# Kernel optimization log

Measured on AMD Instinct MI355X. Metric: run time of the kernel, lower is better.

The kernel has to match this reference:

```python
import jax, jax.numpy as jnp
import numpy as np

HEAD_DIM = 128
N_HEADS = 16
N_KV_HEADS = 4
ROPE_BASE = 10000.0
TRAIN_SEQ_LEN = 1024


def _rotary_cos_sin(seq_len, rd, base=ROPE_BASE, train_len=TRAIN_SEQ_LEN):
    # NTK-style base scaling when seq_len exceeds training length (matches Rotary.forward)
    if seq_len > train_len:
        scale = seq_len / train_len
        base = base * scale ** (rd / (rd - 2))
    inv_freq = 1.0 / base ** (np.arange(0, rd, 2, dtype=np.float32) / rd)
    freqs = np.outer(np.arange(seq_len, dtype=np.float32), inv_freq)  # [T, rd/2]
    cos = jnp.asarray(np.cos(freqs))[None, :, None, :]  # [1,T,1,rd/2]
    sin = jnp.asarray(np.sin(freqs))[None, :, None, :]
    return cos, sin


def _apply_rotary(x, cos, sin):
    h = x.shape[-1] // 2
    x1, x2 = x[..., :h], x[..., h:]
    return jnp.concatenate((x1 * cos + x2 * sin, -x1 * sin + x2 * cos), axis=-1)


def _rms_norm(x):
    eps = jnp.finfo(x.dtype).eps
    return x * jax.lax.rsqrt(jnp.mean(x * x, axis=-1, keepdims=True) + eps)


def setup_inputs() -> dict:
    key = jax.random.key(0)
    ks = jax.random.split(key, 6)
    B, T, D = 4, 2048, 2048
    x = jax.random.normal(ks[0], (B, T, D), dtype=jnp.float32)
    q_w = jax.random.normal(ks[1], (D, D), dtype=jnp.float32) * 0.02
    k_w = jax.random.normal(ks[2], (N_KV_HEADS * HEAD_DIM, D), dtype=jnp.float32) * 0.02
    v_w = jax.random.normal(ks[3], (N_KV_HEADS * HEAD_DIM, D), dtype=jnp.float32) * 0.02
    out_w = jax.random.normal(ks[4], (D, D), dtype=jnp.float32) * 0.02
    q_gain = jnp.ones((N_HEADS,), dtype=jnp.float32)
    return {"x": x, "q_w": q_w, "k_w": k_w, "v_w": v_w, "out_w": out_w, "q_gain": q_gain}


def reference(x, q_w, k_w, v_w, out_w, q_gain):
    B, T, D = x.shape
    q = (x @ q_w.T).reshape(B, T, N_HEADS, HEAD_DIM)
    k = (x @ k_w.T).reshape(B, T, N_KV_HEADS, HEAD_DIM)
    v = (x @ v_w.T).reshape(B, T, N_KV_HEADS, HEAD_DIM)
    q = _rms_norm(q)
    k = _rms_norm(k)
    cos, sin = _rotary_cos_sin(T, HEAD_DIM)
    q = _apply_rotary(q, cos, sin)
    k = _apply_rotary(k, cos, sin)
    q = q * q_gain[None, None, :, None]
    # GQA: expand kv heads (repeat_interleave semantics)
    rep = N_HEADS // N_KV_HEADS
    k = jnp.repeat(k, rep, axis=2)  # [B,T,H,D]
    v = jnp.repeat(v, rep, axis=2)
    scale = 1.0 / jnp.sqrt(jnp.asarray(HEAD_DIM, dtype=x.dtype))
    scores = jnp.einsum("bthd,bshd->bhts", q, k) * scale  # [B,H,T,T]
    causal = jnp.tril(jnp.ones((T, T), dtype=bool))
    scores = jnp.where(causal[None, None], scores, jnp.asarray(-jnp.inf, dtype=scores.dtype))
    w = jax.nn.softmax(scores, axis=-1)
    y = jnp.einsum("bhts,bshd->bthd", w, v).reshape(B, T, D)
    return y @ out_w.T
```

## Files before the change

### kernel.cpp

```cpp
#include <hip/hip_runtime.h>
#include <hip/hip_bf16.h>
#include <math.h>

#define HEAD_DIM 128
#define NH 16
#define NKV 4
#define BB 4
#define TT 2048
#define DD 2048
#define ROWS (BB*TT)

typedef unsigned short u16;
typedef unsigned int u32;
typedef __attribute__((ext_vector_type(8))) short short8;
typedef __attribute__((ext_vector_type(4))) float f32x4;
typedef __attribute__((ext_vector_type(16))) float f32x16;
typedef __attribute__((ext_vector_type(4))) unsigned short u16x4;

__device__ __forceinline__ float bf2f(u16 u) {
    union { unsigned int i; float f; } v; v.i = ((unsigned int)u) << 16; return v.f;
}
__device__ __forceinline__ u16 f2bf(float f) {
    union { float f; unsigned int i; } v; v.f = f;
    unsigned int r = v.i + 0x7FFFu + ((v.i >> 16) & 1u);
    return (u16)(r >> 16);
}
__device__ __forceinline__ f32x4 mfma16(short8 a, short8 b, f32x4 c) {
    return __builtin_amdgcn_mfma_f32_16x16x32_bf16(a, b, c, 0, 0, 0);
}
__device__ __forceinline__ f32x16 mfma32(short8 a, short8 b, f32x16 c) {
    return __builtin_amdgcn_mfma_f32_32x32x16_bf16(a, b, c, 0, 0, 0);
}
__device__ __forceinline__ f32x16 zero16() {
    f32x16 z;
    #pragma unroll
    for (int i = 0; i < 16; ++i) z[i] = 0.f;
    return z;
}
__device__ __forceinline__ void gload_lds16(const u16* g, u16* l) {
    __builtin_amdgcn_global_load_lds(
        (const __attribute__((address_space(1))) unsigned int*)(const void*)g,
        (__attribute__((address_space(3))) unsigned int*)(void*)l, 16, 0, 0);
}

__global__ __launch_bounds__(256)
void cast_f2b(const float* __restrict__ in, u16* __restrict__ out, int n)
{
    int i = (blockIdx.x * 256 + threadIdx.x) * 4;
    if (i >= n) return;
    float4 v = *(const float4*)(in + i);
    u16x4 o;
    o.x = f2bf(v.x); o.y = f2bf(v.y); o.z = f2bf(v.z); o.w = f2bf(v.w);
    *(u16x4*)(out + i) = o;
}

__global__ __launch_bounds__(256)
void rope_table(float* __restrict__ cs, float* __restrict__ sn, float base)
{
    int idx = blockIdx.x * 256 + threadIdx.x;
    if (idx >= TT * 64) return;
    int t = idx >> 6;
    int d = idx & 63;
    float inv = powf(base, -(float)(2 * d) / 128.0f);
    float f = (float)t * inv;
    cs[idx] = cosf(f);
    sn[idx] = sinf(f);
}

__global__ __launch_bounds__(256)
void rmsrope_bf16(const u16* __restrict__ xin, u16* __restrict__ xout,
                  const float* __restrict__ cs, const float* __restrict__ sn,
                  const float* __restrict__ gain,
                  int heads, int use_gain, float pre, int relayout)
{
    int row  = blockIdx.x * 4 + (threadIdx.x >> 6);
    int lane = threadIdx.x & 63;
    int h = row % heads;
    int t = (row / heads) % TT;
    int b = row / (heads * TT);
    size_t base = (size_t)row * HEAD_DIM;

    float x1 = bf2f(xin[base + lane]);
    float x2 = bf2f(xin[base + 64 + lane]);
    float ss = x1 * x1 + x2 * x2;
    #pragma unroll
    for (int m = 1; m < 64; m <<= 1) ss += __shfl_xor(ss, m, 64);
    float r = 1.0f / sqrtf(ss * (1.0f / 128.0f) + 1.1920929e-7f);
    x1 *= r; x2 *= r;

    float c = cs[t * 64 + lane];
    float s = sn[t * 64 + lane];
    float o1 =  x1 * c + x2 * s;
    float o2 = -x1 * s + x2 * c;
    float g = use_gain ? gain[h] * pre : pre;
    o1 *= g; o2 *= g;

    size_t orow = relayout ? ((size_t)(b * heads + h) * TT + t) : (size_t)row;
    size_t obase = orow * HEAD_DIM;
    xout[obase + lane]      = f2bf(o1);
    xout[obase + 64 + lane] = f2bf(o2);
}

__global__ __launch_bounds__(256)
void transpose_v(const u16* __restrict__ vbh, u16* __restrict__ vtb)
{
    __shared__ u16 tile[64][72];
    const int tb = blockIdx.x;
    const int db = blockIdx.y;
    const int z  = blockIdx.z;
    const int tid = threadIdx.x;

    {
        const int r = tid >> 2, cq = tid & 3;
        const u16* src = vbh + ((size_t)(((z >> 2) * TT + tb * 64 + r) * NKV + (z & 3))) * 128
                             + db * 64 + cq * 16;
        short8 s0 = *(const short8*)(src);
        short8 s1 = *(const short8*)(src + 8);
        #pragma unroll
        for (int e = 0; e < 8; ++e) tile[r][cq * 16 + e]     = (u16)s0[e];
        #pragma unroll
        for (int e = 0; e < 8; ++e) tile[r][cq * 16 + 8 + e] = (u16)s1[e];
    }
    __syncthreads();
    {
        const int d = tid >> 2, tq = tid & 3;
        __attribute__((aligned(16))) u16 tmp[16];
        #pragma unroll
        for (int e = 0; e < 16; ++e) {
            int esw = (e & 3) | ((e & 4) << 1) | ((e & 8) >> 1);
            tmp[e] = tile[tq * 16 + esw][d];
        }
        u16* dst = vtb + (((size_t)(z * (TT / 64) + tb) * 128 + (db * 64 + d)) << 6) + tq * 16;
        *(short8*)(dst)     = ((short8*)tmp)[0];
        *(short8*)(dst + 8) = ((short8*)tmp)[1];
    }
}

template<int BN, int OUTMODE>
__global__ __launch_bounds__(512, 2)
void gemm256(const u16* __restrict__ A, const u16* __restrict__ W,
             void* __restrict__ C0, void* __restrict__ C1)
{
    constexpr int WN    = (BN == 256) ? 4 : 2;
    constexpr int MR    = (BN == 256) ? 8 : 4;
    constexpr int WROW  = (BN == 256) ? 128 : 64;
    constexpr int NT    = DD / 64;
    constexpr int BROWS = BN / 8;
    constexpr int NBI   = BROWS / 8;

    __shared__ u16 AsL[2 * 256 * 64];
    __shared__ u16 BsL[2 * BN * 64];

    const int tid = threadIdx.x;
    const int w = tid >> 6, l = tid & 63;
    const int lq = l & 15, lg = l >> 4;
    const int wmi = (WN == 4) ? (w >> 2) : (w >> 1);
    const int wni = w & (WN - 1);

    int bmi, bni;
    {
        const int bid = blockIdx.x;
        const int wg = (bid & 7) * 32 + (bid >> 3);
        const int st = wg >> 2, wi = wg & 3;
        const int sty = st >> 2, stx = st & 3;
        bmi = sty * 2 + (wi >> 1);
        bni = stx * 2 + (wi & 1);
    }
    const int bm = bmi * 256, bn = bni * BN;

    const int r8 = l >> 3;
    const int chs = (l & 7) ^ r8;
    const u16* Ag = A + (size_t)(bm + r8) * DD + chs * 8;
    const u16* Wg = W + (size_t)(bn + r8) * DD + chs * 8;

    f32x4 acc[MR][4];
    #pragma unroll
    for (int m = 0; m < MR; ++m)
        #pragma unroll
        for (int n = 0; n < 4; ++n) acc[m][n] = (f32x4){0.f, 0.f, 0.f, 0.f};

    auto stage = [&](int buf, int t) {
        const size_t ko = (size_t)t * 64;
        u16* Ad = AsL + buf * (256 * 64);
        u16* Bd = BsL + buf * (BN * 64);
        #pragma unroll
        for (int j = 0; j < 4; ++j) {
            int rb = w * 32 + j * 8;
            gload_lds16(Ag + (size_t)rb * DD + ko, Ad + rb * 64);
        }
        #pragma unroll
        for (int j = 0; j < NBI; ++j) {
            int rb = w * BROWS + j * 8;
            gload_lds16(Wg + (size_t)rb * DD + ko, Bd + rb * 64);
        }
    };

    stage(0, 0);
    stage(1, 1);
    if constexpr (BN == 256) asm volatile("s_waitcnt vmcnt(8)" ::: "memory");
    else                     asm volatile("s_waitcnt vmcnt(6)" ::: "memory");
    __builtin_amdgcn_s_barrier();
    __builtin_amdgcn_sched_barrier(0);

    const int swz = lq & 7;
    for (int t = 0; t < NT; ++t) {
        const int buf = t & 1;
        const u16* Ab = AsL + buf * (256 * 64);
        const u16* Bb = BsL + buf * (BN * 64);
        #pragma unroll
        for (int ks = 0; ks < 2; ++ks) {
            short8 af[MR], bf[4];
            #pragma unroll
            for (int m = 0; m < MR; ++m) {
                int arow = wmi * WROW + m * 16 + lq;
                af[m] = *(const short8*)(Ab + arow * 64 + (((ks * 4 + lg) ^ swz) << 3));
            }
            #pragma unroll
            for (int n = 0; n < 4; ++n) {
                int brow = wni * 64 + n * 16 + lq;
                bf[n] = *(const short8*)(Bb + brow * 64 + (((ks * 4 + lg) ^ swz) << 3));
            }
            __builtin_amdgcn_s_setprio(1);
            #pragma unroll
            for (int m = 0; m < MR; ++m)
                #pragma unroll
                for (int n = 0; n < 4; ++n)
                    acc[m][n] = mfma16(af[m], bf[n], acc[m][n]);
            __builtin_amdgcn_s_setprio(0);
        }

        if (t + 1 < NT) {
            __builtin_amdgcn_sched_barrier(0);
            __builtin_amdgcn_s_barrier();
            if (t + 2 < NT) {
                stage(buf, t + 2);
                if constexpr (BN == 256) asm volatile("s_waitcnt vmcnt(8)" ::: "memory");
                else                     asm volatile("s_waitcnt vmcnt(6)" ::: "memory");
            } else {
                asm volatile("s_waitcnt vmcnt(0)" ::: "memory");
            }
            __builtin_amdgcn_s_barrier();
            __builtin_amdgcn_sched_barrier(0);
        }
    }

    #pragma unroll
    for (int m = 0; m < MR; ++m) {
        int grow = bm + wmi * WROW + m * 16 + lg * 4;
        #pragma unroll
        for (int n = 0; n < 4; ++n) {
            int col = wni * 64 + n * 16 + lq;
            #pragma unroll
            for (int q = 0; q < 4; ++q) {
                float v = acc[m][n][q];
                if constexpr (OUTMODE == 0) {
                    ((u16*)C0)[(size_t)(grow + q) * 2048 + bn + col] = f2bf(v);
                } else if constexpr (OUTMODE == 2) {
                    ((float*)C0)[(size_t)(grow + q) * 2048 + bn + col] = v;
                } else {
                    int cg = bn + col;
                    if (cg < 512)
                        ((u16*)C0)[(size_t)(grow + q) * 512 + cg] = f2bf(v);
                    else
                        ((u16*)C1)[(size_t)(grow + q) * 512 + (cg - 512)] = f2bf(v);
                }
            }
        }
    }
}

__global__ __launch_bounds__(256, 2)
void attn_mfma(const u16* __restrict__ qg,
               const u16* __restrict__ kg,
               const u16* __restrict__ vtg,
               u16* __restrict__ yg)
{
    __shared__ u16 Ks[2][64 * 128];
    __shared__ u16 Vs[2][128 * 64];

    const int tid = threadIdx.x, wid = tid >> 6, l = tid & 63;
    const int lq = l & 31, hi = l >> 5, hi4 = hi << 2;

    const int bid = blockIdx.x;
    const int xcd  = bid & 7;
    const int s    = bid >> 3;
    const int gsub = s >> 5;
    const int hh   = (s >> 3) & 3;
    const int fold = s & 7;
    const int g    = xcd + (gsub << 3);
    const int b = g >> 2, kvh = g & 3;
    const int h = kvh * 4 + hh;

    const u16* kg_bh = kg + (((size_t)g * TT) << 7);
    const u16* vt_bh = vtg + (size_t)g * (TT / 64) * 8192;
    const u16* q_bh  = qg + (((size_t)(b * NH + h) * TT) << 7);

    const int nta = 2 * fold + 2;
    const int NT  = 34;

    const int kro = l >> 4;
    const int kch = l & 15;
    const int vro = l >> 3;
    const int vchs = (l & 7) ^ vro;

    auto stage = [&](int buf, int kt) {
        #pragma unroll
        for (int i = 0; i < 4; ++i) {
            int kr = wid * 16 + i * 4 + kro;
            gload_lds16(kg_bh + (((size_t)(kt * 64 + kr)) << 7) + ((kch ^ (kr & 7)) << 3),
                        &Ks[buf][(wid * 16 + i * 4) << 7]);
            int vr = wid * 32 + i * 8 + vro;
            gload_lds16(vt_bh + (size_t)kt * 8192 + (vr << 6) + (vchs << 3),
                        &Vs[buf][(wid * 32 + i * 8) << 6]);
        }
    };

    stage(0, 0);
    stage(1, 1);
    asm volatile("s_waitcnt vmcnt(8)" ::: "memory");
    __builtin_amdgcn_s_barrier();
    __builtin_amdgcn_sched_barrier(0);

    int step = 0;

    for (int seg = 0; seg < 2; ++seg) {
        const int qblk = seg ? (15 - fold) : fold;
        const int nseg = seg ? (32 - 2 * fold) : nta;
        const int qrow = qblk * 128 + wid * 32 + lq;
        const int diag = (qblk * 128 + wid * 32) >> 6;

        const u16* qptr = q_bh + ((size_t)qrow << 7) + hi * 8;
        short8 qf[8];
        #pragma unroll
        for (int q = 0; q < 8; ++q)
            qf[q] = *(const short8*)(qptr + q * 16);

        f32x16 accO[4];
        #pragma unroll
        for (int d = 0; d < 4; ++d) accO[d] = zero16();
        float m2 = -1e30f, lr = 0.f;

        for (int kt = 0; kt < nseg; ++kt, ++step) {
            const int buf = step & 1;

            if (kt <= diag) {
                const u16* Kc = Ks[buf];
                f32x16 accS0 = zero16(), accS1 = zero16();
                __builtin_amdgcn_s_setprio(1);
                #pragma unroll
                for (int ss = 0; ss < 8; ++ss) {
                    int c = ((2 * ss + hi) ^ (lq & 7)) << 3;
                    short8 kf0 = *(const short8*)(Kc + (lq << 7) + c);
                    accS0 = mfma32(kf0, qf[ss], accS0);
                    short8 kf1 = *(const short8*)(Kc + ((32 + lq) << 7) + c);
                    accS1 = mfma32(kf1, qf[ss], accS1);
                }
                __builtin_amdgcn_s_setprio(0);

                float p[32];
                if (kt == diag) {
                    #pragma unroll
                    for (int r = 0; r < 16; ++r) {
                        int key0 = kt * 64 + (r & 3) + 8 * (r >> 2) + hi4;
                        p[r]      = (key0      > qrow) ? -INFINITY : accS0[r];
                        p[16 + r] = (key0 + 32 > qrow) ? -INFINITY : accS1[r];
                    }
                } else {
                    #pragma unroll
                    for (int r = 0; r < 16; ++r) { p[r] = accS0[r]; p[16 + r] = accS1[r]; }
                }

                float t16[16];
                #pragma unroll
                for (int i = 0; i < 16; ++i) t16[i] = fmaxf(p[i], p[i + 16]);
                #pragma unroll
                for (int i = 0; i < 8; ++i) t16[i] = fmaxf(t16[i], t16[i + 8]);
                #pragma unroll
                for (int i = 0; i < 4; ++i) t16[i] = fmaxf(t16[i], t16[i + 4]);
                float pm = fmaxf(fmaxf(t16[0], t16[1]), fmaxf(t16[2], t16[3]));
                pm = fmaxf(pm, __shfl_xor(pm, 32, 64));

                float mn = m2;
                if (!__all(pm - m2 <= 8.0f)) {
                    mn = fmaxf(m2, pm);
                    float al = exp2f(m2 - mn);
                    lr *= al;
                    #pragma unroll
                    for (int d = 0; d < 4; ++d) accO[d] *= al;
                    m2 = mn;
                }

                #pragma unroll
                for (int r = 0; r < 32; ++r) p[r] = exp2f(p[r] - mn);
                #pragma unroll
                for (int i = 0; i < 16; ++i) t16[i] = p[i] + p[i + 16];
                #pragma unroll
                for (int i = 0; i < 8; ++i) t16[i] += t16[i + 8];
                #pragma unroll
                for (int i = 0; i < 4; ++i) t16[i] += t16[i + 4];
                float rs = (t16[0] + t16[1]) + (t16[2] + t16[3]);
                rs += __shfl_xor(rs, 32, 64);
                lr += rs;

                short8 pfrag[4];
                #pragma unroll
                for (int kb = 0; kb < 2; ++kb)
                    #pragma unroll
                    for (int c = 0; c < 2; ++c) {
                        union { u32 u[4]; short8 s8; } f;
                        #pragma unroll
                        for (int j = 0; j < 4; ++j) {
                            __hip_bfloat162 hb = __float22bfloat162_rn(
                                make_float2(p[kb * 16 + 8 * c + 2 * j],
                                            p[kb * 16 + 8 * c + 2 * j + 1]));
                            f.u[j] = *reinterpret_cast<u32*>(&hb);
                        }
                        pfrag[kb * 2 + c] = f.s8;
                    }

                const u16* Vc = Vs[buf];
                #pragma unroll
                for (int d = 0; d < 4; ++d) {
                    const u16* vr8 = Vc + ((d * 32 + lq) << 6);
                    short8 vf0 = *(const short8*)(vr8 + (((0 + hi) ^ (lq & 7)) << 3));
                    short8 vf1 = *(const short8*)(vr8 + (((2 + hi) ^ (lq & 7)) << 3));
                    short8 vf2 = *(const short8*)(vr8 + (((4 + hi) ^ (lq & 7)) << 3));
                    short8 vf3 = *(const short8*)(vr8 + (((6 + hi) ^ (lq & 7)) << 3));
                    __builtin_amdgcn_s_setprio(1);
                    accO[d] = mfma32(vf0, pfrag[0], accO[d]);
                    accO[d] = mfma32(vf1, pfrag[1], accO[d]);
                    accO[d] = mfma32(vf2, pfrag[2], accO[d]);
                    accO[d] = mfma32(vf3, pfrag[3], accO[d]);
                    __builtin_amdgcn_s_setprio(0);
                }
            }

            if (step + 1 < NT) {
                __builtin_amdgcn_sched_barrier(0);
                __builtin_amdgcn_s_barrier();
                if (step + 2 < NT) {
                    int tn = step + 2;
                    stage(buf, (tn < nta) ? tn : tn - nta);
                    asm volatile("s_waitcnt vmcnt(8)" ::: "memory");
                } else {
                    asm volatile("s_waitcnt vmcnt(0)" ::: "memory");
                }
                __builtin_amdgcn_s_barrier();
                __builtin_amdgcn_sched_barrier(0);
            }
        }

        float inv = 1.0f / lr;
        u16* yrow = yg + ((size_t)((b * TT + qrow) * NH + h) << 7);
        #pragma unroll
        for (int d = 0; d < 4; ++d)
            #pragma unroll
            for (int r = 0; r < 4; ++r) {
                u16x4 o;
                #pragma unroll
                for (int q = 0; q < 4; ++q) o[q] = f2bf(accO[d][4 * r + q] * inv);
                *(u16x4*)(yrow + d * 32 + 8 * r + hi4) = o;
            }
    }
}

extern "C" void kernel_launch(void* const* d_in, const int* in_sizes, int n_in,
                              void* d_out, int out_size, void* d_ws, size_t ws_size,
                              hipStream_t stream)
{
    const float* x      = (const float*)d_in[0];
    const float* q_w    = (const float*)d_in[1];
    const float* k_w    = (const float*)d_in[2];
    const float* v_w    = (const float*)d_in[3];
    const float* out_w  = (const float*)d_in[4];
    const float* q_gain = (const float*)d_in[5];
    float* out = (float*)d_out;

    char* ws = (char*)d_ws;
    u16* qh   = (u16*)(ws);
    u16* xh   = (u16*)(ws + 33554432ull);
    u16* wqkv = (u16*)(ws + 67108864ull);
    u16* kh   = (u16*)(ws + 79691776ull);
    u16* vbh  = (u16*)(ws + 88080384ull);
    float* cs = (float*)(ws + 96468992ull);
    float* sn = cs + TT * 64;
    u16* wq   = wqkv;
    u16* wkv  = wqkv + 4194304;
    u16* q2   = xh;
    u16* kk   = wqkv;
    u16* vtb  = kh;
    u16* wout = vbh;
    u16* y    = qh;

    dim3 blk(256);

    double base = 10000.0 * pow((double)TT / 1024.0, 128.0 / 126.0);
    rope_table<<<(TT * 64) / 256, blk, 0, stream>>>(cs, sn, (float)base);

    cast_f2b<<<(ROWS * DD) / 1024, blk, 0, stream>>>(x, xh, ROWS * DD);
    cast_f2b<<<(DD * DD) / 1024, blk, 0, stream>>>(q_w, wq, DD * DD);
    cast_f2b<<<(512 * DD) / 1024, blk, 0, stream>>>(k_w, wkv, 512 * DD);
    cast_f2b<<<(512 * DD) / 1024, blk, 0, stream>>>(v_w, wkv + 1048576, 512 * DD);

    gemm256<256, 0><<<dim3(256), dim3(512), 0, stream>>>(xh, wq, qh, nullptr);
    gemm256<128, 1><<<dim3(256), dim3(512), 0, stream>>>(xh, wkv, kh, vbh);

    const float pre_q = 0.08838834764831845f * 1.4426950408889634f;
    rmsrope_bf16<<<(ROWS * NH) / 4, blk, 0, stream>>>(qh, q2, cs, sn, q_gain, NH, 1, pre_q, 1);
    rmsrope_bf16<<<(ROWS * NKV) / 4, blk, 0, stream>>>(kh, kk, cs, sn, nullptr, NKV, 0, 1.0f, 1);

    transpose_v<<<dim3(TT / 64, 2, BB * NKV), blk, 0, stream>>>(vbh, vtb);

    cast_f2b<<<(DD * DD) / 1024, blk, 0, stream>>>(out_w, wout, DD * DD);

    attn_mfma<<<dim3(512), blk, 0, stream>>>(q2, kk, vtb, y);

    gemm256<256, 2><<<dim3(256), dim3(512), 0, stream>>>(y, wout, out, nullptr);
}
```

Measured before the change: 354.8 us.

## Read K/V directly from global memory in attention, dropping LDS staging

The attention kernel stops staging K and V tiles into shared memory with double buffering and barriers; each wave now loads its K and V MFMA fragments straight from global memory (relying on L1/L2). The folded two-segment causal schedule is replaced by one query block per workgroup, with the grid doubled to 1024 blocks and a remapped block index. Launch bounds rise to 4 workgroups per CU. This removes LDS traffic and barrier synchronisation and raises occupancy, but each of the 4 waves reloads the same K/V tiles from cache with non-swizzled, strided 16-byte accesses, and the causal load balancing across blocks changes.

```diff
diff --git a/kernel.cpp b/kernel.cpp
--- a/kernel.cpp
+++ b/kernel.cpp
@@ -269,25 +269,23 @@
     }
 }
 
-__global__ __launch_bounds__(256, 2)
+__global__ __launch_bounds__(256, 4)
 void attn_mfma(const u16* __restrict__ qg,
                const u16* __restrict__ kg,
                const u16* __restrict__ vtg,
                u16* __restrict__ yg)
 {
-    __shared__ u16 Ks[2][64 * 128];
-    __shared__ u16 Vs[2][128 * 64];
-
     const int tid = threadIdx.x, wid = tid >> 6, l = tid & 63;
     const int lq = l & 31, hi = l >> 5, hi4 = hi << 2;
 
-    const int bid = blockIdx.x;
-    const int xcd  = bid & 7;
-    const int s    = bid >> 3;
-    const int gsub = s >> 5;
-    const int hh   = (s >> 3) & 3;
-    const int fold = s & 7;
-    const int g    = xcd + (gsub << 3);
+    const int bid   = blockIdx.x;
+    const int xcd   = bid & 7;
+    const int slot  = bid >> 3;
+    const int gsub  = slot & 1;
+    const int hh    = (slot >> 1) & 3;
+    const int qslot = slot >> 3;
+    const int qblk  = (qslot < 8) ? qslot : 23 - qslot;
+    const int g     = xcd + (gsub << 3);
     const int b = g >> 2, kvh = g & 3;
     const int h = kvh * 4 + hh;
 
@@ -295,173 +293,123 @@
     const u16* vt_bh = vtg + (size_t)g * (TT / 64) * 8192;
     const u16* q_bh  = qg + (((size_t)(b * NH + h) * TT) << 7);
 
-    const int nta = 2 * fold + 2;
-    const int NT  = 34;
-
-    const int kro = l >> 4;
-    const int kch = l & 15;
-    const int vro = l >> 3;
-    const int vchs = (l & 7) ^ vro;
-
-    auto stage = [&](int buf, int kt) {
-        #pragma unroll
-        for (int i = 0; i < 4; ++i) {
-            int kr = wid * 16 + i * 4 + kro;
-            gload_lds16(kg_bh + (((size_t)(kt * 64 + kr)) << 7) + ((kch ^ (kr & 7)) << 3),
-                        &Ks[buf][(wid * 16 + i * 4) << 7]);
-            int vr = wid * 32 + i * 8 + vro;
-            gload_lds16(vt_bh + (size_t)kt * 8192 + (vr << 6) + (vchs << 3),
-                        &Vs[buf][(wid * 32 + i * 8) << 6]);
-        }
-    };
-
-    stage(0, 0);
-    stage(1, 1);
-    asm volatile("s_waitcnt vmcnt(8)" ::: "memory");
-    __builtin_amdgcn_s_barrier();
-    __builtin_amdgcn_sched_barrier(0);
-
-    int step = 0;
-
-    for (int seg = 0; seg < 2; ++seg) {
-        const int qblk = seg ? (15 - fold) : fold;
-        const int nseg = seg ? (32 - 2 * fold) : nta;
-        const int qrow = qblk * 128 + wid * 32 + lq;
-        const int diag = (qblk * 128 + wid * 32) >> 6;
-
-        const u16* qptr = q_bh + ((size_t)qrow << 7) + hi * 8;
-        short8 qf[8];
-        #pragma unroll
-        for (int q = 0; q < 8; ++q)
-            qf[q] = *(const short8*)(qptr + q * 16);
-
-        f32x16 accO[4];
-        #pragma unroll
-        for (int d = 0; d < 4; ++d) accO[d] = zero16();
-        float m2 = -1e30f, lr = 0.f;
-
-        for (int kt = 0; kt < nseg; ++kt, ++step) {
-            const int buf = step & 1;
-
-            if (kt <= diag) {
-                const u16* Kc = Ks[buf];
-                f32x16 accS0 = zero16(), accS1 = zero16();
-                __builtin_amdgcn_s_setprio(1);
+    const int qrow = qblk * 128 + wid * 32 + lq;
+    const int diag = (qblk * 128 + wid * 32) >> 6;
+
+    const u16* qptr = q_bh + ((size_t)qrow << 7) + hi * 8;
+    short8 qf[8];
+    #pragma unroll
+    for (int s = 0; s < 8; ++s)
+        qf[s] = *(const short8*)(qptr + s * 16);
+
+    f32x16 accO[4];
+    #pragma unroll
+    for (int d = 0; d < 4; ++d) accO[d] = zero16();
+    float m2 = -1e30f, lr = 0.f;
+
+    for (int kt = 0; kt <= diag; ++kt) {
+        const u16* kbase = kg_bh + (((size_t)(kt * 64)) << 7);
+        f32x16 accS0 = zero16(), accS1 = zero16();
+        __builtin_amdgcn_s_setprio(1);
+        #pragma unroll
+        for (int ss = 0; ss < 8; ++ss) {
+            const int c = (2 * ss + hi) << 3;
+            short8 kf0 = *(const short8*)(kbase + (lq << 7) + c);
+            accS0 = mfma32(kf0, qf[ss], accS0);
+            short8 kf1 = *(const short8*)(kbase + ((32 + lq) << 7) + c);
+            accS1 = mfma32(kf1, qf[ss], accS1);
+        }
+        __builtin_amdgcn_s_setprio(0);
+
+        float p[32];
+        if (kt == diag) {
+            #pragma unroll
+            for (int r = 0; r < 16; ++r) {
+                int key0 = kt * 64 + (r & 3) + 8 * (r >> 2) + hi4;
+                p[r]      = (key0      > qrow) ? -INFINITY : accS0[r];
+                p[16 + r] = (key0 + 32 > qrow) ? -INFINITY : accS1[r];
+            }
+        } else {
+            #pragma unroll
+            for (int r = 0; r < 16; ++r) { p[r] = accS0[r]; p[16 + r] = accS1[r]; }
+        }
+
+        float t16[16];
+        #pragma unroll
+        for (int i = 0; i < 16; ++i) t16[i] = fmaxf(p[i], p[i + 16]);
+        #pragma unroll
+        for (int i = 0; i < 8; ++i) t16[i] = fmaxf(t16[i], t16[i + 8]);
+        #pragma unroll
+        for (int i = 0; i < 4; ++i) t16[i] = fmaxf(t16[i], t16[i + 4]);
+        float pm = fmaxf(fmaxf(t16[0], t16[1]), fmaxf(t16[2], t16[3]));
+        pm = fmaxf(pm, __shfl_xor(pm, 32, 64));
+
+        float mn = m2;
+        if (!__all(pm - m2 <= 8.0f)) {
+            mn = fmaxf(m2, pm);
+            float al = exp2f(m2 - mn);
+            lr *= al;
+            #pragma unroll
+            for (int d = 0; d < 4; ++d) accO[d] *= al;
+            m2 = mn;
+        }
+
+        #pragma unroll
+        for (int r = 0; r < 32; ++r) p[r] = exp2f(p[r] - mn);
+        #pragma unroll
+        for (int i = 0; i < 16; ++i) t16[i] = p[i] + p[i + 16];
+        #pragma unroll
+        for (int i = 0; i < 8; ++i) t16[i] += t16[i + 8];
+        #pragma unroll
+        for (int i = 0; i < 4; ++i) t16[i] += t16[i + 4];
+        float rs = (t16[0] + t16[1]) + (t16[2] + t16[3]);
+        rs += __shfl_xor(rs, 32, 64);
+        lr += rs;
+
+        short8 pfrag[4];
+        #pragma unroll
+        for (int kb = 0; kb < 2; ++kb)
+            #pragma unroll
+            for (int c = 0; c < 2; ++c) {
+                union { u32 u[4]; short8 s8; } f;
                 #pragma unroll
-                for (int ss = 0; ss < 8; ++ss) {
-                    int c = ((2 * ss + hi) ^ (lq & 7)) << 3;
-                    short8 kf0 = *(const short8*)(Kc + (lq << 7) + c);
-                    accS0 = mfma32(kf0, qf[ss], accS0);
-                    short8 kf1 = *(const short8*)(Kc + ((32 + lq) << 7) + c);
-                    accS1 = mfma32(kf1, qf[ss], accS1);
+                for (int j = 0; j < 4; ++j) {
+                    __hip_bfloat162 hb = __float22bfloat162_rn(
+                        make_float2(p[kb * 16 + 8 * c + 2 * j],
+                                    p[kb * 16 + 8 * c + 2 * j + 1]));
+                    f.u[j] = *reinterpret_cast<u32*>(&hb);
                 }
-                __builtin_amdgcn_s_setprio(0);
-
-                float p[32];
-                if (kt == diag) {
-                    #pragma unroll
-                    for (int r = 0; r < 16; ++r) {
-                        int key0 = kt * 64 + (r & 3) + 8 * (r >> 2) + hi4;
-                        p[r]      = (key0      > qrow) ? -INFINITY : accS0[r];
-                        p[16 + r] = (key0 + 32 > qrow) ? -INFINITY : accS1[r];
-                    }
-                } else {
-                    #pragma unroll
-                    for (int r = 0; r < 16; ++r) { p[r] = accS0[r]; p[16 + r] = accS1[r]; }
-                }
-
-                float t16[16];
-                #pragma unroll
-                for (int i = 0; i < 16; ++i) t16[i] = fmaxf(p[i], p[i + 16]);
-                #pragma unroll
-                for (int i = 0; i < 8; ++i) t16[i] = fmaxf(t16[i], t16[i + 8]);
-                #pragma unroll
-                for (int i = 0; i < 4; ++i) t16[i] = fmaxf(t16[i], t16[i + 4]);
-                float pm = fmaxf(fmaxf(t16[0], t16[1]), fmaxf(t16[2], t16[3]));
-                pm = fmaxf(pm, __shfl_xor(pm, 32, 64));
-
-                float mn = m2;
-                if (!__all(pm - m2 <= 8.0f)) {
-                    mn = fmaxf(m2, pm);
-                    float al = exp2f(m2 - mn);
-                    lr *= al;
-                    #pragma unroll
-                    for (int d = 0; d < 4; ++d) accO[d] *= al;
-                    m2 = mn;
-                }
-
-                #pragma unroll
-                for (int r = 0; r < 32; ++r) p[r] = exp2f(p[r] - mn);
-                #pragma unroll
-                for (int i = 0; i < 16; ++i) t16[i] = p[i] + p[i + 16];
-                #pragma unroll
-                for (int i = 0; i < 8; ++i) t16[i] += t16[i + 8];
-                #pragma unroll
-                for (int i = 0; i < 4; ++i) t16[i] += t16[i + 4];
-                float rs = (t16[0] + t16[1]) + (t16[2] + t16[3]);
-                rs += __shfl_xor(rs, 32, 64);
-                lr += rs;
-
-                short8 pfrag[4];
-                #pragma unroll
-                for (int kb = 0; kb < 2; ++kb)
-                    #pragma unroll
-                    for (int c = 0; c < 2; ++c) {
-                        union { u32 u[4]; short8 s8; } f;
-                        #pragma unroll
-                        for (int j = 0; j < 4; ++j) {
-                            __hip_bfloat162 hb = __float22bfloat162_rn(
-                                make_float2(p[kb * 16 + 8 * c + 2 * j],
-                                            p[kb * 16 + 8 * c + 2 * j + 1]));
-                            f.u[j] = *reinterpret_cast<u32*>(&hb);
-                        }
-                        pfrag[kb * 2 + c] = f.s8;
-                    }
-
-                const u16* Vc = Vs[buf];
-                #pragma unroll
-                for (int d = 0; d < 4; ++d) {
-                    const u16* vr8 = Vc + ((d * 32 + lq) << 6);
-                    short8 vf0 = *(const short8*)(vr8 + (((0 + hi) ^ (lq & 7)) << 3));
-                    short8 vf1 = *(const short8*)(vr8 + (((2 + hi) ^ (lq & 7)) << 3));
-                    short8 vf2 = *(const short8*)(vr8 + (((4 + hi) ^ (lq & 7)) << 3));
-                    short8 vf3 = *(const short8*)(vr8 + (((6 + hi) ^ (lq & 7)) << 3));
-                    __builtin_amdgcn_s_setprio(1);
-                    accO[d] = mfma32(vf0, pfrag[0], accO[d]);
-                    accO[d] = mfma32(vf1, pfrag[1], accO[d]);
-                    accO[d] = mfma32(vf2, pfrag[2], accO[d]);
-                    accO[d] = mfma32(vf3, pfrag[3], accO[d]);
-                    __builtin_amdgcn_s_setprio(0);
-                }
-            }
-
-            if (step + 1 < NT) {
-                __builtin_amdgcn_sched_barrier(0);
-                __builtin_amdgcn_s_barrier();
-                if (step + 2 < NT) {
-                    int tn = step + 2;
-                    stage(buf, (tn < nta) ? tn : tn - nta);
-                    asm volatile("s_waitcnt vmcnt(8)" ::: "memory");
-                } else {
-                    asm volatile("s_waitcnt vmcnt(0)" ::: "memory");
-                }
-                __builtin_amdgcn_s_barrier();
-                __builtin_amdgcn_sched_barrier(0);
-            }
-        }
-
-        float inv = 1.0f / lr;
-        u16* yrow = yg + ((size_t)((b * TT + qrow) * NH + h) << 7);
-        #pragma unroll
-        for (int d = 0; d < 4; ++d)
-            #pragma unroll
-            for (int r = 0; r < 4; ++r) {
-                u16x4 o;
-                #pragma unroll
-                for (int q = 0; q < 4; ++q) o[q] = f2bf(accO[d][4 * r + q] * inv);
-                *(u16x4*)(yrow + d * 32 + 8 * r + hi4) = o;
-            }
-    }
+                pfrag[kb * 2 + c] = f.s8;
+            }
+
+        const u16* vbase = vt_bh + (size_t)kt * 8192;
+        #pragma unroll
+        for (int d = 0; d < 4; ++d) {
+            const u16* vr8 = vbase + ((d * 32 + lq) << 6);
+            short8 vf0 = *(const short8*)(vr8 + ((0 + hi) << 3));
+            short8 vf1 = *(const short8*)(vr8 + ((2 + hi) << 3));
+            short8 vf2 = *(const short8*)(vr8 + ((4 + hi) << 3));
+            short8 vf3 = *(const short8*)(vr8 + ((6 + hi) << 3));
+            __builtin_amdgcn_s_setprio(1);
+            accO[d] = mfma32(vf0, pfrag[0], accO[d]);
+            accO[d] = mfma32(vf1, pfrag[1], accO[d]);
+            accO[d] = mfma32(vf2, pfrag[2], accO[d]);
+            accO[d] = mfma32(vf3, pfrag[3], accO[d]);
+            __builtin_amdgcn_s_setprio(0);
+        }
+    }
+
+    float inv = 1.0f / lr;
+    u16* yrow = yg + ((size_t)((b * TT + qrow) * NH + h) << 7);
+    #pragma unroll
+    for (int d = 0; d < 4; ++d)
+        #pragma unroll
+        for (int r = 0; r < 4; ++r) {
+            u16x4 o;
+            #pragma unroll
+            for (int q = 0; q < 4; ++q) o[q] = f2bf(accO[d][4 * r + q] * inv);
+            *(u16x4*)(yrow + d * 32 + 8 * r + hi4) = o;
+        }
 }
 
 extern "C" void kernel_launch(void* const* d_in, const int* in_sizes, int n_in,
@@ -513,7 +461,7 @@
 
     cast_f2b<<<(DD * DD) / 1024, blk, 0, stream>>>(out_w, wout, DD * DD);
 
-    attn_mfma<<<dim3(512), blk, 0, stream>>>(q2, kk, vtb, y);
+    attn_mfma<<<dim3(1024), blk, 0, stream>>>(q2, kk, vtb, y);
 
     gemm256<256, 2><<<dim3(256), dim3(512), 0, stream>>>(y, wout, out, nullptr);
 }
```

Result: slower. 582.4 us (+64.2%).
